# Kernel optimization log

Measured on AMD Instinct MI355X. Metric: run time of the kernel, lower is better.

## Reference

```python
import jax, jax.numpy as jnp
import numpy as np

B, S, D = 4, 2048, 1024
H = 16
DH = D // H

def setup_inputs() -> dict:
    key = jax.random.key(0)
    ks = jax.random.split(key, 5)
    s = 1.0 / np.sqrt(D)
    return {
        "inputs": jax.random.normal(ks[0], (B, S, D), dtype=jnp.float32),
        "Wq": jax.random.normal(ks[1], (D, D), dtype=jnp.float32) * s,
        "Wk": jax.random.normal(ks[2], (D, D), dtype=jnp.float32) * s,
        "Wv": jax.random.normal(ks[3], (D, D), dtype=jnp.float32) * s,
        "Wo": jax.random.normal(ks[4], (D, D), dtype=jnp.float32) * s,
        "bo": jnp.zeros((D,), dtype=jnp.float32),
    }

def reference(inputs, Wq, Wk, Wv, Wo, bo):
    b, s, _ = inputs.shape
    # nn.Linear: y = x @ W.T (no bias for QKV)
    Q = (inputs @ Wq.T).reshape(b, s, H, DH)
    K = (inputs @ Wk.T).reshape(b, s, H, DH)
    V = (inputs @ Wv.T).reshape(b, s, H, DH)
    scores = jnp.einsum("bqhd,bkhd->bhqk", Q, K)  # [B,H,S,S]
    causal = jnp.triu(jnp.ones((s, s), dtype=bool), k=1)
    scores = jnp.where(causal, -jnp.inf, scores)
    w = jax.nn.softmax(scores / np.sqrt(DH), axis=-1)  # dropout p=0.0 -> identity
    Z = jnp.einsum("bhqk,bkhd->bqhd", w, V).reshape(b, s, D)
    return Z @ Wo.T + bo
```

## Files before the change

### kernel.cpp

```cpp
#include <hip/hip_runtime.h>
#include <hip/hip_bf16.h>


#define Bq 4
#define Sq 2048
#define Dq 1024
#define Hq 16
#define DHq 64

typedef __attribute__((ext_vector_type(8))) short short8;
typedef __attribute__((ext_vector_type(4))) float f32x4;
typedef __attribute__((ext_vector_type(4))) unsigned short ushort4v;
typedef __attribute__((ext_vector_type(2))) unsigned int uint2v;

static __device__ __forceinline__ unsigned short f2bfu(float f) {
    union { __hip_bfloat16 h; unsigned short u; } cv;
    cv.h = __float2bfloat16(f);
    return cv.u;
}
static __device__ __forceinline__ unsigned int cvtpk(float lo, float hi) {
    unsigned int r;
    asm("v_cvt_pk_bf16_f32 %0, %1, %2" : "=v"(r) : "v"(lo), "v"(hi));
    return r;
}

__global__ __launch_bounds__(256) void tobf16(
    const float* __restrict__ X, const float* __restrict__ W0,
    const float* __restrict__ W1, const float* __restrict__ W2,
    const float* __restrict__ W3,
    unsigned short* __restrict__ xb, unsigned short* __restrict__ wb)
{
    const size_t i = ((size_t)blockIdx.x * 256 + threadIdx.x) * 8;
    const size_t NX = (size_t)8388608;
    const float* src; unsigned short* dst; size_t off;
    if (i < NX) { src = X; dst = xb; off = i; }
    else {
        const size_t j = i - NX;
        const int w = (int)(j >> 20);
        off = j & 1048575;
        src = (w == 0) ? W0 : (w == 1) ? W1 : (w == 2) ? W2 : W3;
        dst = wb + ((size_t)w << 20);
    }
    const float4 a = *reinterpret_cast<const float4*>(src + off);
    const float4 b = *reinterpret_cast<const float4*>(src + off + 4);
    short8 v;
    v[0] = (short)f2bfu(a.x); v[1] = (short)f2bfu(a.y);
    v[2] = (short)f2bfu(a.z); v[3] = (short)f2bfu(a.w);
    v[4] = (short)f2bfu(b.x); v[5] = (short)f2bfu(b.y);
    v[6] = (short)f2bfu(b.z); v[7] = (short)f2bfu(b.w);
    *reinterpret_cast<short8*>(dst + off) = v;
}



__global__ __launch_bounds__(256) void mm_qkv(
    const unsigned short* __restrict__ Ab, const unsigned short* __restrict__ Wall,
    unsigned short* __restrict__ oq, unsigned short* __restrict__ ok,
    unsigned short* __restrict__ ovt)
{
    __shared__ unsigned short As[128 * 64];
    __shared__ unsigned short Bs[128 * 64];

    const int z = blockIdx.z;
    const unsigned short* W = Wall + ((size_t)z << 20);

    const int m0 = blockIdx.x * 128, n0 = blockIdx.y * 128;
    const int t = threadIdx.x, lane = t & 63, wave = t >> 6;
    const int g = lane >> 4, c = lane & 15;
    const int wm = wave >> 1, wn = wave & 1;
    const int r8 = lane >> 3, c8 = lane & 7;
    const int ss = (c8 ^ (r8 & 7)) * 8;

    f32x4 acc[4][4] = {};

    for (int kt = 0; kt < 16; ++kt) {
        const int kb = kt * 64;
#pragma unroll
        for (int p = 0; p < 4; ++p) {
            const int rowb = wave * 8 + p * 32;
            const unsigned short* ga = Ab + (size_t)(m0 + rowb + r8) * 1024 + kb + ss;
            const unsigned short* gb = W  + (size_t)(n0 + rowb + r8) * 1024 + kb + ss;
            __builtin_amdgcn_global_load_lds(
                (const __attribute__((address_space(1))) unsigned int*)ga,
                (__attribute__((address_space(3))) unsigned int*)(As + rowb * 64), 16, 0, 0);
            __builtin_amdgcn_global_load_lds(
                (const __attribute__((address_space(1))) unsigned int*)gb,
                (__attribute__((address_space(3))) unsigned int*)(Bs + rowb * 64), 16, 0, 0);
        }
        __syncthreads();
        if (z != 2) {
#pragma unroll
            for (int ks = 0; ks < 2; ++ks) {
                const int sa = ((ks * 4 + g) ^ (c & 7)) * 8;
                short8 bf[4];
#pragma unroll
                for (int nt = 0; nt < 4; ++nt)
                    bf[nt] = *reinterpret_cast<const short8*>(&Bs[(wn * 64 + nt * 16 + c) * 64 + sa]);
#pragma unroll
                for (int mt = 0; mt < 4; ++mt) {
                    const short8 af = *reinterpret_cast<const short8*>(&As[(wm * 64 + mt * 16 + c) * 64 + sa]);
#pragma unroll
                    for (int nt = 0; nt < 4; ++nt)
                        acc[mt][nt] = __builtin_amdgcn_mfma_f32_16x16x32_bf16(af, bf[nt], acc[mt][nt], 0, 0, 0);
                }
            }
        } else {
#pragma unroll
            for (int ks = 0; ks < 2; ++ks) {
                const int sa = ((ks * 4 + g) ^ (c & 7)) * 8;
                short8 bf[4];
#pragma unroll
                for (int nt = 0; nt < 4; ++nt)
                    bf[nt] = *reinterpret_cast<const short8*>(&Bs[(wn * 64 + nt * 16 + c) * 64 + sa]);
#pragma unroll
                for (int mt = 0; mt < 4; ++mt) {
                    const short8 af = *reinterpret_cast<const short8*>(&As[(wm * 64 + mt * 16 + c) * 64 + sa]);
#pragma unroll
                    for (int nt = 0; nt < 4; ++nt)
                        acc[mt][nt] = __builtin_amdgcn_mfma_f32_16x16x32_bf16(bf[nt], af, acc[mt][nt], 0, 0, 0);
                }
            }
        }
        __syncthreads();
    }

    if (z == 2) {
#pragma unroll
        for (int mt = 0; mt < 4; ++mt)
#pragma unroll
            for (int nt = 0; nt < 4; ++nt)
#pragma unroll
                for (int r = 0; r < 4; ++r) {
                    const int m = m0 + wm * 64 + mt * 16 + c;
                    const int n = n0 + wn * 64 + nt * 16 + g * 4 + r;
                    const int bb = m >> 11, s = m & 2047;
                    const int h = n >> 6, d = n & 63;
                    const size_t off = (size_t)(bb * Hq + h) * 131072
                        + (s >> 6) * 4096 + ((d >> 4) & 3) * 1024 + ((s >> 5) & 1) * 512
                        + ((s >> 3) & 3) * 128 + (d & 15) * 8 + (s & 7);
                    ovt[off] = f2bfu(acc[mt][nt][r]);
                }
    } else {
        const float oscale = (z == 0) ? 0.180336880f : 1.0f;
        unsigned short* out = z ? ok : oq;
#pragma unroll
        for (int mt = 0; mt < 4; ++mt)
#pragma unroll
            for (int nt = 0; nt < 4; ++nt)
#pragma unroll
                for (int r = 0; r < 4; ++r) {
                    const int m = m0 + wm * 64 + mt * 16 + g * 4 + r;
                    const int n = n0 + wn * 64 + nt * 16 + c;
                    const int bb = m >> 11, s = m & 2047;
                    const int h = n >> 6, d = n & 63;
                    const size_t off = (size_t)(bb * Hq + h) * 131072
                        + (s >> 4) * 1024 + (d >> 5) * 512 + ((d >> 3) & 3) * 128
                        + (s & 15) * 8 + (d & 7);
                    out[off] = f2bfu(acc[mt][nt][r] * oscale);
                }
    }
}

static __device__ __forceinline__ void qtile(
    const short8* kf, const short8* vf, const short8 q0, const short8 q1,
    int rel, int g, int c, unsigned short (*PtW)[72],
    f32x4* oacc, f32x4& lacc, const short8 onesf)
{
    f32x4 st[4] = {};
#pragma unroll
    for (int k2 = 0; k2 < 4; ++k2) {
        st[k2] = __builtin_amdgcn_mfma_f32_16x16x32_bf16(kf[2 * k2],     q0, st[k2], 0, 0, 0);
        st[k2] = __builtin_amdgcn_mfma_f32_16x16x32_bf16(kf[2 * k2 + 1], q1, st[k2], 0, 0, 0);
    }

    if (rel < 4) {
        const int lim = rel * 16 + c;
#pragma unroll
        for (int kt = 0; kt < 4; ++kt)
#pragma unroll
            for (int r = 0; r < 4; ++r)
                if (kt * 16 + g * 4 + r > lim) st[kt][r] = -3.0e38f;
    }

#pragma unroll
    for (int kt = 0; kt < 4; ++kt) {
        uint2v u;
        u[0] = cvtpk(exp2f(st[kt][0]), exp2f(st[kt][1]));
        u[1] = cvtpk(exp2f(st[kt][2]), exp2f(st[kt][3]));
        *reinterpret_cast<uint2v*>(&PtW[c][kt * 16 + g * 4]) = u;
    }
    const short8 pb0 = *reinterpret_cast<const short8*>(&PtW[c][g * 8]);
    const short8 pb1 = *reinterpret_cast<const short8*>(&PtW[c][32 + g * 8]);

#pragma unroll
    for (int dt = 0; dt < 4; ++dt) {
        oacc[dt] = __builtin_amdgcn_mfma_f32_16x16x32_bf16(vf[2 * dt],     pb0, oacc[dt], 0, 0, 0);
        oacc[dt] = __builtin_amdgcn_mfma_f32_16x16x32_bf16(vf[2 * dt + 1], pb1, oacc[dt], 0, 0, 0);
    }
    lacc = __builtin_amdgcn_mfma_f32_16x16x32_bf16(onesf, pb0, lacc, 0, 0, 0);
    lacc = __builtin_amdgcn_mfma_f32_16x16x32_bf16(onesf, pb1, lacc, 0, 0, 0);
}

#define ATTN_STEP(KC, KN, IB)                                                   \
  {                                                                             \
    short8 vf[8];                                                               \
    {                                                                           \
      const unsigned short* vp = Vb + (size_t)(IB) * 4096 + lane * 8;           \
      _Pragma("unroll")                                                         \
      for (int i = 0; i < 8; ++i) vf[i] = *reinterpret_cast<const short8*>(vp + i * 512); \
    }                                                                           \
    if ((IB) < ibmax) {                                                         \
      const unsigned short* kp = Kb + (size_t)((IB) + 1) * 4096 + lane * 8;     \
      _Pragma("unroll")                                                         \
      for (int i = 0; i < 8; ++i) KN[i] = *reinterpret_cast<const short8*>(kp + i * 512); \
    }                                                                           \
    __builtin_amdgcn_sched_barrier(0);                                          \
    if ((IB) <= 2 * qi)                                                         \
      qtile(KC, vf, qA0, qA1, qtA - 4 * (IB), g, c, Pt[wave][0], oA, lA, onesf);\
    qtile(KC, vf, qB0, qB1, qtB - 4 * (IB), g, c, Pt[wave][1], oB, lB, onesf);  \
  }

__global__ __launch_bounds__(256) void attn(
    const unsigned short* __restrict__ Qf, const unsigned short* __restrict__ Kf,
    const unsigned short* __restrict__ Vf, unsigned short* __restrict__ O)
{
    __shared__ unsigned short Pt[4][2][16][72];

    const int bid = blockIdx.x;
    const int pair = (bid >> 3) & 7;
    const int bh = (bid & 7) | ((bid >> 6) << 3);

    const int t = threadIdx.x, lane = t & 63, wave = t >> 6;
    const int g = lane >> 4, c = lane & 15;
    const size_t base = (size_t)bh * (Sq * DHq);
    const unsigned short* Qb = Qf + base;
    const unsigned short* Kb = Kf + base;
    const unsigned short* Vb = Vf + base;
    const int b = bh >> 4, h = bh & 15;

    short8 onesf;
#pragma unroll
    for (int j = 0; j < 8; ++j) onesf[j] = (short)0x3F80;

#pragma unroll 1
    for (int pp = 0; pp < 2; ++pp) {
        const int qi = pp ? (15 - pair) : pair;
        const int qtA = qi * 8 + wave;
        const int qtB = qtA + 4;

        const unsigned short* qpA = Qb + (size_t)qtA * 1024 + lane * 8;
        const unsigned short* qpB = Qb + (size_t)qtB * 1024 + lane * 8;
        const short8 qA0 = *reinterpret_cast<const short8*>(qpA);
        const short8 qA1 = *reinterpret_cast<const short8*>(qpA + 512);
        const short8 qB0 = *reinterpret_cast<const short8*>(qpB);
        const short8 qB1 = *reinterpret_cast<const short8*>(qpB + 512);

        f32x4 oA[4] = {}, oB[4] = {};
        f32x4 lA = {}, lB = {};

        const int ibmax = 2 * qi + 1;

        short8 ka[8], kb2[8];
        {
            const unsigned short* kp = Kb + lane * 8;
#pragma unroll
            for (int i = 0; i < 8; ++i) ka[i] = *reinterpret_cast<const short8*>(kp + i * 512);
        }
        int ib = 0;
        for (;;) {
            ATTN_STEP(ka, kb2, ib); if (ib == ibmax) break; ++ib;
            ATTN_STEP(kb2, ka, ib); if (ib == ibmax) break; ++ib;
        }

        const float rlA = 1.0f / lA[0];
        const float rlB = 1.0f / lB[0];
        const size_t orowA = ((size_t)b * Sq + qtA * 16 + c) * Dq + h * 64;
        const size_t orowB = ((size_t)b * Sq + qtB * 16 + c) * Dq + h * 64;
#pragma unroll
        for (int dt = 0; dt < 4; ++dt) {
            uint2v uA, uB;
            uA[0] = cvtpk(oA[dt][0] * rlA, oA[dt][1] * rlA);
            uA[1] = cvtpk(oA[dt][2] * rlA, oA[dt][3] * rlA);
            uB[0] = cvtpk(oB[dt][0] * rlB, oB[dt][1] * rlB);
            uB[1] = cvtpk(oB[dt][2] * rlB, oB[dt][3] * rlB);
            *reinterpret_cast<uint2v*>(&O[orowA + dt * 16 + g * 4]) = uA;
            *reinterpret_cast<uint2v*>(&O[orowB + dt * 16 + g * 4]) = uB;
        }
    }
}

__global__ __launch_bounds__(256) void mm_o(
    const unsigned short* __restrict__ Ab, const unsigned short* __restrict__ Wall,
    const float* __restrict__ bo, float* __restrict__ outf)
{
    __shared__ unsigned short As[128 * 64];
    __shared__ unsigned short Bs[128 * 64];

    const unsigned short* W = Wall + ((size_t)3 << 20);

    const int m0 = blockIdx.x * 128, n0 = blockIdx.y * 128;
    const int t = threadIdx.x, lane = t & 63, wave = t >> 6;
    const int g = lane >> 4, c = lane & 15;
    const int wm = wave >> 1, wn = wave & 1;
    const int r8 = lane >> 3, c8 = lane & 7;
    const int ss = (c8 ^ (r8 & 7)) * 8;

    f32x4 acc[4][4] = {};

    for (int kt = 0; kt < 16; ++kt) {
        const int kb = kt * 64;
#pragma unroll
        for (int p = 0; p < 4; ++p) {
            const int rowb = wave * 8 + p * 32;
            const unsigned short* ga = Ab + (size_t)(m0 + rowb + r8) * 1024 + kb + ss;
            const unsigned short* gb = W  + (size_t)(n0 + rowb + r8) * 1024 + kb + ss;
            __builtin_amdgcn_global_load_lds(
                (const __attribute__((address_space(1))) unsigned int*)ga,
                (__attribute__((address_space(3))) unsigned int*)(As + rowb * 64), 16, 0, 0);
            __builtin_amdgcn_global_load_lds(
                (const __attribute__((address_space(1))) unsigned int*)gb,
                (__attribute__((address_space(3))) unsigned int*)(Bs + rowb * 64), 16, 0, 0);
        }
        __syncthreads();
#pragma unroll
        for (int ks = 0; ks < 2; ++ks) {
            const int sa = ((ks * 4 + g) ^ (c & 7)) * 8;
            short8 bf[4];
#pragma unroll
            for (int nt = 0; nt < 4; ++nt)
                bf[nt] = *reinterpret_cast<const short8*>(&Bs[(wn * 64 + nt * 16 + c) * 64 + sa]);
#pragma unroll
            for (int mt = 0; mt < 4; ++mt) {
                const short8 af = *reinterpret_cast<const short8*>(&As[(wm * 64 + mt * 16 + c) * 64 + sa]);
#pragma unroll
                for (int nt = 0; nt < 4; ++nt)
                    acc[mt][nt] = __builtin_amdgcn_mfma_f32_16x16x32_bf16(af, bf[nt], acc[mt][nt], 0, 0, 0);
            }
        }
        __syncthreads();
    }

#pragma unroll
    for (int nt = 0; nt < 4; ++nt) {
        const int n = n0 + wn * 64 + nt * 16 + c;
        const float bias = bo[n];
#pragma unroll
        for (int mt = 0; mt < 4; ++mt)
#pragma unroll
            for (int r = 0; r < 4; ++r) {
                const int m = m0 + wm * 64 + mt * 16 + g * 4 + r;
                outf[(size_t)m * 1024 + n] = acc[mt][nt][r] + bias;
            }
    }
}

extern "C" void kernel_launch(void* const* d_in, const int* in_sizes, int n_in,
                              void* d_out, int out_size, void* d_ws, size_t ws_size,
                              hipStream_t stream) {
    const float* X  = (const float*)d_in[0];
    const float* Wq = (const float*)d_in[1];
    const float* Wk = (const float*)d_in[2];
    const float* Wv = (const float*)d_in[3];
    const float* Wo = (const float*)d_in[4];
    const float* bo = (const float*)d_in[5];
    float* out = (float*)d_out;

    const size_t elems = (size_t)Bq * Hq * Sq * DHq;
    unsigned short* q  = (unsigned short*)d_ws;
    unsigned short* k  = q + elems;
    unsigned short* vt = k + elems;
    unsigned short* xo = vt + elems;
    unsigned short* wb = xo + elems;

    tobf16<<<dim3(6144), 256, 0, stream>>>(X, Wq, Wk, Wv, Wo, xo, wb);

    mm_qkv<<<dim3(64, 8, 3), 256, 0, stream>>>(xo, wb, q, k, vt);

    attn<<<dim3(512), 256, 0, stream>>>(q, k, vt, xo);

    mm_o<<<dim3(64, 8, 1), 256, 0, stream>>>(xo, wb, bo, out);
}
```

Measured before the change: 194.8 us.

## Stage K/V blocks into LDS with async global loads, double-buffered, 8-wave blocks

```diff
diff --git a/kernel.cpp b/kernel.cpp
--- a/kernel.cpp
+++ b/kernel.cpp
@@ -161,6 +161,19 @@
     }
 }
 
+static __device__ __forceinline__ void stage_kv8(
+    const unsigned short* __restrict__ Kb, const unsigned short* __restrict__ Vb,
+    int kb, unsigned short* kl, unsigned short* vl, int wave, int lane)
+{
+    const int off = wave * 512 + lane * 8;
+    __builtin_amdgcn_global_load_lds(
+        (const __attribute__((address_space(1))) unsigned int*)(Kb + (size_t)kb * 4096 + off),
+        (__attribute__((address_space(3))) unsigned int*)(kl + wave * 512), 16, 0, 0);
+    __builtin_amdgcn_global_load_lds(
+        (const __attribute__((address_space(1))) unsigned int*)(Vb + (size_t)kb * 4096 + off),
+        (__attribute__((address_space(3))) unsigned int*)(vl + wave * 512), 16, 0, 0);
+}
+
 static __device__ __forceinline__ void qtile(
     const short8* kf, const short8* vf, const short8 q0, const short8 q1,
     int rel, int g, int c, unsigned short (*PtW)[72],
@@ -201,34 +214,17 @@
     lacc = __builtin_amdgcn_mfma_f32_16x16x32_bf16(onesf, pb1, lacc, 0, 0, 0);
 }
 
-#define ATTN_STEP(KC, KN, IB)                                                   \
-  {                                                                             \
-    short8 vf[8];                                                               \
-    {                                                                           \
-      const unsigned short* vp = Vb + (size_t)(IB) * 4096 + lane * 8;           \
-      _Pragma("unroll")                                                         \
-      for (int i = 0; i < 8; ++i) vf[i] = *reinterpret_cast<const short8*>(vp + i * 512); \
-    }                                                                           \
-    if ((IB) < ibmax) {                                                         \
-      const unsigned short* kp = Kb + (size_t)((IB) + 1) * 4096 + lane * 8;     \
-      _Pragma("unroll")                                                         \
-      for (int i = 0; i < 8; ++i) KN[i] = *reinterpret_cast<const short8*>(kp + i * 512); \
-    }                                                                           \
-    __builtin_amdgcn_sched_barrier(0);                                          \
-    if ((IB) <= 2 * qi)                                                         \
-      qtile(KC, vf, qA0, qA1, qtA - 4 * (IB), g, c, Pt[wave][0], oA, lA, onesf);\
-    qtile(KC, vf, qB0, qB1, qtB - 4 * (IB), g, c, Pt[wave][1], oB, lB, onesf);  \
-  }
-
-__global__ __launch_bounds__(256) void attn(
+__global__ __launch_bounds__(512) void attn(
     const unsigned short* __restrict__ Qf, const unsigned short* __restrict__ Kf,
     const unsigned short* __restrict__ Vf, unsigned short* __restrict__ O)
 {
-    __shared__ unsigned short Pt[4][2][16][72];
+    __shared__ unsigned short Kl[2][4096];
+    __shared__ unsigned short Vl[2][4096];
+    __shared__ unsigned short Pt[8][2][16][72];
 
     const int bid = blockIdx.x;
-    const int pair = (bid >> 3) & 7;
-    const int bh = (bid & 7) | ((bid >> 6) << 3);
+    const int pair = (bid >> 3) & 3;
+    const int bh = (bid & 7) | ((bid >> 5) << 3);
 
     const int t = threadIdx.x, lane = t & 63, wave = t >> 6;
     const int g = lane >> 4, c = lane & 15;
@@ -244,9 +240,12 @@
 
 #pragma unroll 1
     for (int pp = 0; pp < 2; ++pp) {
-        const int qi = pp ? (15 - pair) : pair;
-        const int qtA = qi * 8 + wave;
-        const int qtB = qtA + 4;
+        const int qi = pp ? (3 - pair) + 4 : pair;
+        const int qi2 = pp ? (7 - pair) : pair;
+        const int qq = qi2;
+        const int qtA = qq * 16 + wave * 2;
+        const int qtB = qtA + 1;
+        (void)qi;
 
         const unsigned short* qpA = Qb + (size_t)qtA * 1024 + lane * 8;
         const unsigned short* qpB = Qb + (size_t)qtB * 1024 + lane * 8;
@@ -258,18 +257,32 @@
         f32x4 oA[4] = {}, oB[4] = {};
         f32x4 lA = {}, lB = {};
 
-        const int ibmax = 2 * qi + 1;
-
-        short8 ka[8], kb2[8];
-        {
-            const unsigned short* kp = Kb + lane * 8;
-#pragma unroll
-            for (int i = 0; i < 8; ++i) ka[i] = *reinterpret_cast<const short8*>(kp + i * 512);
-        }
-        int ib = 0;
-        for (;;) {
-            ATTN_STEP(ka, kb2, ib); if (ib == ibmax) break; ++ib;
-            ATTN_STEP(kb2, ka, ib); if (ib == ibmax) break; ++ib;
+        const int ibmax = 4 * qq + 3;
+
+        stage_kv8(Kb, Vb, 0, Kl[0], Vl[0], wave, lane);
+        __syncthreads();
+
+#pragma unroll 1
+        for (int ib = 0; ib <= ibmax; ++ib) {
+            const int cur = ib & 1;
+            if (ib < ibmax)
+                stage_kv8(Kb, Vb, ib + 1, Kl[cur ^ 1], Vl[cur ^ 1], wave, lane);
+            __builtin_amdgcn_sched_barrier(0);
+
+            if (4 * ib <= qtB) {
+                short8 kf[8], vf[8];
+#pragma unroll
+                for (int i = 0; i < 8; ++i)
+                    kf[i] = *reinterpret_cast<const short8*>(&Kl[cur][lane * 8 + i * 512]);
+#pragma unroll
+                for (int i = 0; i < 8; ++i)
+                    vf[i] = *reinterpret_cast<const short8*>(&Vl[cur][lane * 8 + i * 512]);
+
+                if (4 * ib <= qtA)
+                    qtile(kf, vf, qA0, qA1, qtA - 4 * ib, g, c, Pt[wave][0], oA, lA, onesf);
+                qtile(kf, vf, qB0, qB1, qtB - 4 * ib, g, c, Pt[wave][1], oB, lB, onesf);
+            }
+            __syncthreads();
         }
 
         const float rlA = 1.0f / lA[0];
@@ -376,7 +389,7 @@
 
     mm_qkv<<<dim3(64, 8, 3), 256, 0, stream>>>(xo, wb, q, k, vt);
 
-    attn<<<dim3(512), 256, 0, stream>>>(q, k, vt, xo);
+    attn<<<dim3(256), 512, 0, stream>>>(q, k, vt, xo);
 
     mm_o<<<dim3(64, 8, 1), 256, 0, stream>>>(xo, wb, bo, out);
 }
```

New measurement: 187.5 us. 1.04x faster.
